# Kernel optimization log

Measured on AMD Instinct MI355X. Metric: run time of the kernel, lower is better.

## Reference

```python
import jax, jax.numpy as jnp
import numpy as np

B, S, D_IN, D_ATT = 8, 2048, 512, 512

def setup_inputs() -> dict:
    key = jax.random.key(0)
    ks = jax.random.split(key, 7)
    sc = 1.0 / np.sqrt(D_IN)
    return {
        "x": jax.random.normal(ks[0], (B, S, D_IN), dtype=jnp.float32),
        "Wq": jax.random.uniform(ks[1], (D_IN, D_ATT), jnp.float32, -sc, sc),
        "bq": jax.random.uniform(ks[2], (D_ATT,), jnp.float32, -sc, sc),
        "Wk": jax.random.uniform(ks[3], (D_IN, D_ATT), jnp.float32, -sc, sc),
        "bk": jax.random.uniform(ks[4], (D_ATT,), jnp.float32, -sc, sc),
        "Wv": jax.random.uniform(ks[5], (D_IN, D_ATT), jnp.float32, -sc, sc),
        "bv": jax.random.uniform(ks[6], (D_ATT,), jnp.float32, -sc, sc),
    }

def reference(x, Wq, bq, Wk, bk, Wv, bv):
    # Linear projections: [B, S, D_att]
    q = jnp.einsum("bsd,de->bse", x, Wq) + bq
    k = jnp.einsum("bsd,de->bse", x, Wk) + bk
    v = jnp.einsum("bsd,de->bse", x, Wv) + bv
    # Full scores matrix [B, S, S]; note: NO 1/sqrt(d) scaling in original.
    scores = jnp.einsum("bqe,bke->bqk", q, k)
    attn = jax.nn.softmax(scores, axis=-1)
    return jnp.einsum("bqk,bke->bqe", attn, v)
```

## Files before the change

kernel.cpp:

```cpp
#include <hip/hip_runtime.h>
#include <cstdint>
#include <cstddef>


#define SEQ 2048
#define DIM 512
#define NB 8
#define BSZ (NB * SEQ)
#define KT 64
#define NT (SEQ / KT)

typedef __attribute__((ext_vector_type(8))) _Float16 half8;
typedef __attribute__((ext_vector_type(4))) _Float16 half4;
typedef __attribute__((ext_vector_type(2))) __fp16 fp16x2;
typedef __attribute__((ext_vector_type(4))) float f32x4;
typedef __attribute__((ext_vector_type(16))) float f32x16;

__device__ __forceinline__ unsigned short f2h(float f) {
  _Float16 h = (_Float16)f;
  return __builtin_bit_cast(unsigned short, h);
}
__device__ __forceinline__ half8 ld_frag(const unsigned short* p) {
  return *(const half8*)(const void*)p;
}
__device__ __forceinline__ void gl_lds16(const unsigned short* g, unsigned short* l) {
  __builtin_amdgcn_global_load_lds(
      (__attribute__((address_space(1))) void*)g,
      (__attribute__((address_space(3))) void*)l, 16, 0, 0);
}
__device__ __forceinline__ void bar_vm0() {
  asm volatile("s_waitcnt vmcnt(0)\ns_barrier" ::: "memory");
}
__device__ __forceinline__ void bar_lgkm() {
  asm volatile("s_waitcnt lgkmcnt(0)\ns_barrier" ::: "memory");
}
__device__ __forceinline__ void bar_lgkm_vm0() {
  asm volatile("s_waitcnt lgkmcnt(0) vmcnt(0)\ns_barrier" ::: "memory");
}

__global__ __launch_bounds__(256) void cvt_x_kernel(
    const float* __restrict__ X, unsigned short* __restrict__ xh)
{
  size_t i0 = ((size_t)blockIdx.x * 256 + threadIdx.x) * 8;
  float4 a = *(const float4*)&X[i0];
  float4 b = *(const float4*)&X[i0 + 4];
  ushort4 o0; o0.x = f2h(a.x); o0.y = f2h(a.y); o0.z = f2h(a.z); o0.w = f2h(a.w);
  ushort4 o1; o1.x = f2h(b.x); o1.y = f2h(b.y); o1.z = f2h(b.z); o1.w = f2h(b.w);
  *(ushort4*)&xh[i0] = o0;
  *(ushort4*)&xh[i0 + 4] = o1;
}

__global__ __launch_bounds__(256) void cvt_w_kernel(
    const float* __restrict__ Wq, const float* __restrict__ Wk,
    const float* __restrict__ Wv, unsigned short* __restrict__ Wt)
{
  const int z = blockIdx.z;
  const float* W = (z == 0) ? Wq : (z == 1) ? Wk : Wv;
  unsigned short* out = Wt + (size_t)z * DIM * DIM;
  const int k0 = blockIdx.x * 64, n0 = blockIdx.y * 64;
  const int t = threadIdx.x;
  __shared__ unsigned short tl[64 * 72];
#pragma unroll
  for (int i = 0; i < 4; i++) {
    int f = t + 256 * i;
    int kr = f >> 4, c4 = (f & 15) * 4;
    float4 v = *(const float4*)&W[(size_t)(k0 + kr) * DIM + n0 + c4];
    tl[(c4 + 0) * 72 + kr] = f2h(v.x);
    tl[(c4 + 1) * 72 + kr] = f2h(v.y);
    tl[(c4 + 2) * 72 + kr] = f2h(v.z);
    tl[(c4 + 3) * 72 + kr] = f2h(v.w);
  }
  __syncthreads();
#pragma unroll
  for (int i = 0; i < 2; i++) {
    int f = t + 256 * i;
    int nr = f >> 3, k8 = (f & 7) * 8;
    *(uint4*)&out[(size_t)(n0 + nr) * DIM + k0 + k8] = *(const uint4*)&tl[nr * 72 + k8];
  }
}

__global__ __launch_bounds__(256) void proj_kernel(
    const unsigned short* __restrict__ xh, const unsigned short* __restrict__ Wt,
    const float* __restrict__ bq, const float* __restrict__ bk,
    const float* __restrict__ bv, unsigned short* __restrict__ outbase)
{
  const int z = blockIdx.z;
  const unsigned short* Wz = Wt + (size_t)z * DIM * DIM;
  const float* bias = (z == 0) ? bq : (z == 1) ? bk : bv;
  unsigned short* out = outbase + (size_t)z * BSZ * DIM;
  const int m0 = blockIdx.x * 128, n0 = blockIdx.y * 128;
  const int t = threadIdx.x, lane = t & 63, wave = t >> 6;
  const int wrow = (wave >> 1) * 64, wcol = (wave & 1) * 64;
  const int lr = lane & 15, lq = (lane >> 4) * 8;

  __shared__ unsigned short sm[128 * 132];
  unsigned short* As = sm;
  unsigned short* Bs = sm + 128 * 64;

  f32x4 acc[4][4];
  const f32x4 zero = {0.f, 0.f, 0.f, 0.f};
#pragma unroll
  for (int r = 0; r < 4; r++)
#pragma unroll
    for (int c = 0; c < 4; c++) acc[r][c] = zero;

  for (int k0 = 0; k0 < DIM; k0 += 64) {
    __syncthreads();
#pragma unroll
    for (int i = 0; i < 4; i++) {
      int f = t + 256 * i;
      int row = f >> 3, c8 = (f & 7) * 8;
      gl_lds16(&xh[(size_t)(m0 + row) * DIM + k0 + c8], &As[i * 2048 + wave * 512]);
      gl_lds16(&Wz[(size_t)(n0 + row) * DIM + k0 + c8], &Bs[i * 2048 + wave * 512]);
    }
    __syncthreads();
#pragma unroll
    for (int kk = 0; kk < 64; kk += 32) {
      half8 a[4], b[4];
#pragma unroll
      for (int r = 0; r < 4; r++) a[r] = ld_frag(&As[(wrow + 16 * r + lr) * 64 + kk + lq]);
#pragma unroll
      for (int c = 0; c < 4; c++) b[c] = ld_frag(&Bs[(wcol + 16 * c + lr) * 64 + kk + lq]);
#pragma unroll
      for (int r = 0; r < 4; r++)
#pragma unroll
        for (int c = 0; c < 4; c++)
          acc[r][c] = __builtin_amdgcn_mfma_f32_16x16x32_f16(a[r], b[c], acc[r][c], 0, 0, 0);
    }
  }
  __syncthreads();
#pragma unroll
  for (int c = 0; c < 4; c++) {
    float bb = bias[n0 + wcol + 16 * c + lr];
#pragma unroll
    for (int r = 0; r < 4; r++)
#pragma unroll
      for (int e = 0; e < 4; e++)
        sm[(wrow + 16 * r + (lane >> 4) * 4 + e) * 132 + wcol + 16 * c + lr] =
            f2h(acc[r][c][e] + bb);
  }
  __syncthreads();
#pragma unroll
  for (int i = 0; i < 8; i++) {
    int f = t + 256 * i;
    int row = f >> 4, c8 = (f & 15) * 8;
    *(uint4*)&out[(size_t)(m0 + row) * DIM + n0 + c8] = *(const uint4*)&sm[row * 132 + c8];
  }
}

__global__ __launch_bounds__(256) void vtrans_kernel(
    const unsigned short* __restrict__ vh, unsigned short* __restrict__ vt)
{
  const int b = blockIdx.z;
  const int s0 = blockIdx.x * 64, n0 = blockIdx.y * 64;
  const int t = threadIdx.x;
  __shared__ unsigned short tl[64 * 72];
#pragma unroll
  for (int i = 0; i < 2; i++) {
    int f = t + 256 * i;
    int sr = f >> 3, c8 = (f & 7) * 8;
    uint4 raw = *(const uint4*)&vh[((size_t)b * SEQ + s0 + sr) * DIM + n0 + c8];
    unsigned short u[8];
    *(uint4*)u = raw;
#pragma unroll
    for (int j = 0; j < 8; j++) tl[(c8 + j) * 72 + sr] = u[j];
  }
  __syncthreads();
#pragma unroll
  for (int i = 0; i < 2; i++) {
    int f = t + 256 * i;
    int nr = f >> 3, s8 = (f & 7) * 8;
    *(uint4*)&vt[((size_t)b * DIM + n0 + nr) * SEQ + s0 + s8] = *(const uint4*)&tl[nr * 72 + s8];
  }
}

#define PSTR 68
#define OSTR 516

__global__ __launch_bounds__(256, 1) void flash_kernel(
    const unsigned short* __restrict__ Qb, const unsigned short* __restrict__ Kb,
    const unsigned short* __restrict__ Vtb, float* __restrict__ Ob)
{
  const int zb = blockIdx.x & 7;
  const int q0 = (blockIdx.x >> 3) * 64;
  const unsigned short* Q = Qb + (size_t)zb * SEQ * DIM;
  const unsigned short* K = Kb + (size_t)zb * SEQ * DIM;
  const unsigned short* V = Vtb + (size_t)zb * DIM * SEQ;
  float* Out = Ob + (size_t)zb * SEQ * DIM;

  const int t = threadIdx.x, lane = t & 63, wave = t >> 6;
  const int l31 = lane & 31, hi = lane >> 5;
  const int kh = wave & 1, rh = wave >> 1;
  const int lr = lane & 15, lq4 = lane >> 4;
  const float L2E = 1.4426950408889634f;

  __shared__ unsigned short lds[70664];
  unsigned short* Qbuf = lds;
  unsigned short* Kbuf = lds + 32768;
  unsigned short* Pbuf = lds + 65536;
  float* mpart = (float*)(lds + 65536 + 64 * PSTR);
  float* lpart = mpart + 128;
  float* abuf = lpart + 128;
  float* lrun = abuf + 64;
  unsigned int* fbuf = (unsigned int*)(lrun + 64);

  if (t < 64) lrun[t] = 0.f;

  int koff[16];
#pragma unroll
  for (int i = 0; i < 16; i++) {
    int f = t + 256 * i;
    int row = f >> 6, c = f & 63;
    koff[i] = row * DIM + (c ^ (row & 7)) * 8;
  }

#pragma unroll
  for (int i = 0; i < 16; i++)
    gl_lds16(&Q[(size_t)q0 * DIM + koff[i]], &Qbuf[i * 2048 + wave * 512]);
#pragma unroll
  for (int i = 0; i < 16; i++)
    gl_lds16(&K[koff[i]], &Kbuf[i * 2048 + wave * 512]);

  f32x4 acc[32];
  const f32x4 zero = {0.f, 0.f, 0.f, 0.f};
#pragma unroll
  for (int ob = 0; ob < 32; ob++) acc[ob] = zero;
  float m_run = -__builtin_inff();

  const int keyrow = kh * 32 + l31, ksw = keyrow & 7;
  const int qrow = rh * 32 + l31, qsw = qrow & 7;
  const unsigned short* Kc = Kbuf + keyrow * 512;
  const unsigned short* Qc = Qbuf + qrow * 512;

  for (int kt = 0; kt < NT; kt++) {
    bar_vm0();

    const unsigned short* Vb = V + (size_t)(wave * 128 + lr) * SEQ + kt * KT + lq4 * 8;
    half8 vfA[8];
#pragma unroll
    for (int dc = 0; dc < 4; dc++)
#pragma unroll
      for (int ks = 0; ks < 2; ks++)
        vfA[dc * 2 + ks] = ld_frag(Vb + (size_t)dc * 16 * SEQ + ks * 32);

    f32x16 s0 = {0.f, 0.f, 0.f, 0.f, 0.f, 0.f, 0.f, 0.f,
                 0.f, 0.f, 0.f, 0.f, 0.f, 0.f, 0.f, 0.f};
    f32x16 s1 = s0;
    __builtin_amdgcn_s_setprio(1);
#pragma unroll
    for (int j = 0; j < 16; j++) {
      half8 kf0 = ld_frag(&Kc[((2 * j + hi) ^ ksw) << 3]);
      half8 qv0 = ld_frag(&Qc[((2 * j + hi) ^ qsw) << 3]);
      half8 kf1 = ld_frag(&Kc[((2 * (j + 16) + hi) ^ ksw) << 3]);
      half8 qv1 = ld_frag(&Qc[((2 * (j + 16) + hi) ^ qsw) << 3]);
      s0 = __builtin_amdgcn_mfma_f32_32x32x16_f16(kf0, qv0, s0, 0, 0, 0);
      s1 = __builtin_amdgcn_mfma_f32_32x32x16_f16(kf1, qv1, s1, 0, 0, 0);
    }
    __builtin_amdgcn_s_setprio(0);
    f32x16 sacc = s0 + s1;

    float mx = sacc[0];
#pragma unroll
    for (int i2 = 1; i2 < 16; i2++) mx = fmaxf(mx, sacc[i2]);
    mx = fmaxf(mx, __shfl_xor(mx, 32, 64));
    if (lane < 32) mpart[kh * 64 + rh * 32 + lane] = mx;
    bar_lgkm();

    if (kt + 1 < NT) {
      const unsigned short* Kt = K + (size_t)(kt + 1) * KT * DIM;
#pragma unroll
      for (int i = 0; i < 16; i++)
        gl_lds16(&Kt[koff[i]], &Kbuf[i * 2048 + wave * 512]);
    }
    half8 vfB[8];
#pragma unroll
    for (int dc = 0; dc < 4; dc++)
#pragma unroll
      for (int ks = 0; ks < 2; ks++)
        vfB[dc * 2 + ks] = ld_frag(Vb + (size_t)(dc + 4) * 16 * SEQ + ks * 32);

    float mo = mpart[(kh ^ 1) * 64 + rh * 32 + l31];
    float mxc = fmaxf(mx, mo);
    bool keep = (mxc - m_run <= 8.0f);
    float mnew = keep ? m_run : mxc;
    float alpha = keep ? 1.0f : exp2f((m_run - mnew) * L2E);
    m_run = mnew;
    if (kh == 0 && lane < 32) abuf[rh * 32 + lane] = alpha;
    unsigned long long ball = __ballot(keep);
    if (lane == 0) fbuf[wave] = (ball == ~0ull) ? 1u : 0u;

    float psum = 0.f;
#pragma unroll
    for (int w2 = 0; w2 < 4; w2++) {
      float p0 = exp2f((sacc[4 * w2 + 0] - mnew) * L2E);
      float p1 = exp2f((sacc[4 * w2 + 1] - mnew) * L2E);
      float p2 = exp2f((sacc[4 * w2 + 2] - mnew) * L2E);
      float p3 = exp2f((sacc[4 * w2 + 3] - mnew) * L2E);
      psum += (p0 + p1) + (p2 + p3);
      fp16x2 pa = __builtin_amdgcn_cvt_pkrtz(p0, p1);
      fp16x2 pb = __builtin_amdgcn_cvt_pkrtz(p2, p3);
      unsigned long long both =
          ((unsigned long long)__builtin_bit_cast(unsigned int, pb) << 32) |
          __builtin_bit_cast(unsigned int, pa);
      *(unsigned long long*)&Pbuf[qrow * PSTR + kh * 32 + w2 * 8 + 4 * hi] = both;
    }
    psum += __shfl_xor(psum, 32, 64);
    if (lane < 32) lpart[kh * 64 + rh * 32 + lane] = psum;
    bar_lgkm();
    if (kh == 0 && lane < 32) {
      int r = rh * 32 + lane;
      lrun[r] = alpha * lrun[r] + lpart[r] + lpart[64 + r];
    }

    if (!(fbuf[0] & fbuf[1] & fbuf[2] & fbuf[3])) {
#pragma unroll
      for (int rg = 0; rg < 4; rg++)
#pragma unroll
        for (int e = 0; e < 4; e++) {
          float a = abuf[rg * 16 + lq4 * 4 + e];
#pragma unroll
          for (int dc = 0; dc < 8; dc++) acc[rg * 8 + dc][e] *= a;
        }
    }

    half8 pf[4][2];
#pragma unroll
    for (int rg = 0; rg < 4; rg++)
#pragma unroll
      for (int ks = 0; ks < 2; ks++) {
        const unsigned short* pp = &Pbuf[(rg * 16 + lr) * PSTR + ks * 32 + lq4 * 8];
        half4 lo = *(const half4*)(const void*)pp;
        half4 h2 = *(const half4*)(const void*)(pp + 4);
        half8 v;
#pragma unroll
        for (int q = 0; q < 4; q++) { v[q] = lo[q]; v[4 + q] = h2[q]; }
        pf[rg][ks] = v;
      }
    __builtin_amdgcn_s_setprio(1);
#pragma unroll
    for (int dc = 0; dc < 4; dc++)
#pragma unroll
      for (int rg = 0; rg < 4; rg++) {
        acc[rg * 8 + dc] =
            __builtin_amdgcn_mfma_f32_16x16x32_f16(pf[rg][0], vfA[dc * 2 + 0],
                                                   acc[rg * 8 + dc], 0, 0, 0);
        acc[rg * 8 + dc] =
            __builtin_amdgcn_mfma_f32_16x16x32_f16(pf[rg][1], vfA[dc * 2 + 1],
                                                   acc[rg * 8 + dc], 0, 0, 0);
      }
#pragma unroll
    for (int dc = 4; dc < 8; dc++)
#pragma unroll
      for (int rg = 0; rg < 4; rg++) {
        acc[rg * 8 + dc] =
            __builtin_amdgcn_mfma_f32_16x16x32_f16(pf[rg][0], vfB[(dc - 4) * 2 + 0],
                                                   acc[rg * 8 + dc], 0, 0, 0);
        acc[rg * 8 + dc] =
            __builtin_amdgcn_mfma_f32_16x16x32_f16(pf[rg][1], vfB[(dc - 4) * 2 + 1],
                                                   acc[rg * 8 + dc], 0, 0, 0);
      }
    __builtin_amdgcn_s_setprio(0);
  }

  bar_lgkm_vm0();

  float linv[4][4];
#pragma unroll
  for (int rg = 0; rg < 4; rg++)
#pragma unroll
    for (int e = 0; e < 4; e++) linv[rg][e] = 1.0f / lrun[rg * 16 + lq4 * 4 + e];

  float* Obuf = (float*)lds;
#pragma unroll
  for (int h = 0; h < 2; h++) {
    __syncthreads();
#pragma unroll
    for (int r2 = 0; r2 < 2; r2++) {
      int rg = h * 2 + r2;
#pragma unroll
      for (int e = 0; e < 4; e++) {
        int rowh = r2 * 16 + lq4 * 4 + e;
#pragma unroll
        for (int dc = 0; dc < 8; dc++)
          Obuf[rowh * OSTR + wave * 128 + dc * 16 + lr] = acc[rg * 8 + dc][e] * linv[rg][e];
      }
    }
    __syncthreads();
#pragma unroll
    for (int i = 0; i < 16; i++) {
      int f = t + 256 * i;
      int rowh = f >> 7, c4 = (f & 127) * 4;
      *(float4*)&Out[(size_t)(q0 + h * 32 + rowh) * DIM + c4] =
          *(const float4*)&Obuf[rowh * OSTR + c4];
    }
  }
}

extern "C" void kernel_launch(void* const* d_in, const int* in_sizes, int n_in,
                              void* d_out, int out_size, void* d_ws, size_t ws_size,
                              hipStream_t stream)
{
  const float* X  = (const float*)d_in[0];
  const float* Wq = (const float*)d_in[1];
  const float* bq = (const float*)d_in[2];
  const float* Wk = (const float*)d_in[3];
  const float* bk = (const float*)d_in[4];
  const float* Wv = (const float*)d_in[5];
  const float* bv = (const float*)d_in[6];
  float* Out = (float*)d_out;

  char* ws = (char*)d_ws;
  const size_t MB = 1u << 20;
  unsigned short* qh = (unsigned short*)(ws);
  unsigned short* kh = (unsigned short*)(ws + 16 * MB);
  unsigned short* vh = (unsigned short*)(ws + 32 * MB);
  unsigned short* vt = (unsigned short*)(ws + 48 * MB);
  unsigned short* xh = (unsigned short*)(ws + 48 * MB);
  unsigned short* Wt = (unsigned short*)(ws + 64 * MB);

  cvt_x_kernel<<<dim3(BSZ * DIM / 2048), 256, 0, stream>>>(X, xh);
  cvt_w_kernel<<<dim3(8, 8, 3), 256, 0, stream>>>(Wq, Wk, Wv, Wt);
  proj_kernel<<<dim3(BSZ / 128, DIM / 128, 3), 256, 0, stream>>>(
      xh, Wt, bq, bk, bv, qh);
  vtrans_kernel<<<dim3(SEQ / 64, DIM / 64, NB), 256, 0, stream>>>(vh, vt);
  flash_kernel<<<dim3(NB * SEQ / 64), 256, 0, stream>>>(qh, kh, vt, Out);
}
```

Before: 293.2 us.

## Warp-specialize flash kernel into QK/softmax and PV wave groups with double-buffered P

Doubles the block to 512 threads and splits the waves into two groups. Four waves compute QK scores and the softmax for tile r, while the other four do the PV MFMAs for tile r-1, reading P, alpha and partial sums from double-buffered LDS. The goal is to overlap the softmax and exp work with the PV matrix multiplies instead of running them back to back. It also drops the lazy-rescale threshold and the skip flag, so the accumulator is rescaled every step, and it costs more LDS, more registers per block and one extra pipeline iteration.

```diff
diff --git a/kernel.cpp b/kernel.cpp
--- a/kernel.cpp
+++ b/kernel.cpp
@@ -9,6 +9,7 @@
 #define BSZ (NB * SEQ)
 #define KT 64
 #define NT (SEQ / KT)
+#define QROWS 64
 
 typedef __attribute__((ext_vector_type(8))) _Float16 half8;
 typedef __attribute__((ext_vector_type(4))) _Float16 half4;
@@ -27,9 +28,6 @@
   __builtin_amdgcn_global_load_lds(
       (__attribute__((address_space(1))) void*)g,
       (__attribute__((address_space(3))) void*)l, 16, 0, 0);
-}
-__device__ __forceinline__ void bar_vm0() {
-  asm volatile("s_waitcnt vmcnt(0)\ns_barrier" ::: "memory");
 }
 __device__ __forceinline__ void bar_lgkm() {
   asm volatile("s_waitcnt lgkmcnt(0)\ns_barrier" ::: "memory");
@@ -177,12 +175,12 @@
 #define PSTR 68
 #define OSTR 516
 
-__global__ __launch_bounds__(256, 1) void flash_kernel(
+__global__ __launch_bounds__(512, 1) void flash_kernel(
     const unsigned short* __restrict__ Qb, const unsigned short* __restrict__ Kb,
     const unsigned short* __restrict__ Vtb, float* __restrict__ Ob)
 {
   const int zb = blockIdx.x & 7;
-  const int q0 = (blockIdx.x >> 3) * 64;
+  const int q0 = (blockIdx.x >> 3) * QROWS;
   const unsigned short* Q = Qb + (size_t)zb * SEQ * DIM;
   const unsigned short* K = Kb + (size_t)zb * SEQ * DIM;
   const unsigned short* V = Vtb + (size_t)zb * DIM * SEQ;
@@ -190,41 +188,45 @@
 
   const int t = threadIdx.x, lane = t & 63, wave = t >> 6;
   const int l31 = lane & 31, hi = lane >> 5;
-  const int kh = wave & 1, rh = wave >> 1;
+  const int kh = wave & 1, rh = (wave >> 1) & 1;
+  const int yw = wave & 3;
   const int lr = lane & 15, lq4 = lane >> 4;
   const float L2E = 1.4426950408889634f;
 
-  __shared__ unsigned short lds[70664];
+  __shared__ unsigned short lds[75264];
   unsigned short* Qbuf = lds;
   unsigned short* Kbuf = lds + 32768;
   unsigned short* Pbuf = lds + 65536;
-  float* mpart = (float*)(lds + 65536 + 64 * PSTR);
-  float* lpart = mpart + 128;
-  float* abuf = lpart + 128;
-  float* lrun = abuf + 64;
-  unsigned int* fbuf = (unsigned int*)(lrun + 64);
-
-  if (t < 64) lrun[t] = 0.f;
+  float* mpart = (float*)(lds + 65536 + 2 * 64 * PSTR);
+  float* abuf  = mpart + 128;
+  float* lpart = abuf + 128;
 
   int koff[16];
 #pragma unroll
   for (int i = 0; i < 16; i++) {
-    int f = t + 256 * i;
+    int f = (t & 255) + 256 * i;
     int row = f >> 6, c = f & 63;
     koff[i] = row * DIM + (c ^ (row & 7)) * 8;
   }
 
-#pragma unroll
-  for (int i = 0; i < 16; i++)
-    gl_lds16(&Q[(size_t)q0 * DIM + koff[i]], &Qbuf[i * 2048 + wave * 512]);
-#pragma unroll
-  for (int i = 0; i < 16; i++)
-    gl_lds16(&K[koff[i]], &Kbuf[i * 2048 + wave * 512]);
+  if (wave < 4) {
+#pragma unroll
+    for (int i = 0; i < 16; i++)
+      gl_lds16(&Q[(size_t)q0 * DIM + koff[i]], &Qbuf[i * 2048 + wave * 512]);
+#pragma unroll
+    for (int i = 0; i < 16; i++)
+      gl_lds16(&K[koff[i]], &Kbuf[i * 2048 + wave * 512]);
+  }
 
   f32x4 acc[32];
   const f32x4 zero = {0.f, 0.f, 0.f, 0.f};
 #pragma unroll
   for (int ob = 0; ob < 32; ob++) acc[ob] = zero;
+  float l_y[4][4];
+#pragma unroll
+  for (int rg = 0; rg < 4; rg++)
+#pragma unroll
+    for (int e = 0; e < 4; e++) l_y[rg][e] = 0.f;
   float m_run = -__builtin_inff();
 
   const int keyrow = kh * 32 + l31, ksw = keyrow & 7;
@@ -232,163 +234,168 @@
   const unsigned short* Kc = Kbuf + keyrow * 512;
   const unsigned short* Qc = Qbuf + qrow * 512;
 
-  for (int kt = 0; kt < NT; kt++) {
-    bar_vm0();
-
-    const unsigned short* Vb = V + (size_t)(wave * 128 + lr) * SEQ + kt * KT + lq4 * 8;
-    half8 vfA[8];
-#pragma unroll
-    for (int dc = 0; dc < 4; dc++)
-#pragma unroll
-      for (int ks = 0; ks < 2; ks++)
-        vfA[dc * 2 + ks] = ld_frag(Vb + (size_t)dc * 16 * SEQ + ks * 32);
-
-    f32x16 s0 = {0.f, 0.f, 0.f, 0.f, 0.f, 0.f, 0.f, 0.f,
-                 0.f, 0.f, 0.f, 0.f, 0.f, 0.f, 0.f, 0.f};
-    f32x16 s1 = s0;
-    __builtin_amdgcn_s_setprio(1);
-#pragma unroll
-    for (int j = 0; j < 16; j++) {
-      half8 kf0 = ld_frag(&Kc[((2 * j + hi) ^ ksw) << 3]);
-      half8 qv0 = ld_frag(&Qc[((2 * j + hi) ^ qsw) << 3]);
-      half8 kf1 = ld_frag(&Kc[((2 * (j + 16) + hi) ^ ksw) << 3]);
-      half8 qv1 = ld_frag(&Qc[((2 * (j + 16) + hi) ^ qsw) << 3]);
-      s0 = __builtin_amdgcn_mfma_f32_32x32x16_f16(kf0, qv0, s0, 0, 0, 0);
-      s1 = __builtin_amdgcn_mfma_f32_32x32x16_f16(kf1, qv1, s1, 0, 0, 0);
-    }
-    __builtin_amdgcn_s_setprio(0);
-    f32x16 sacc = s0 + s1;
-
-    float mx = sacc[0];
-#pragma unroll
-    for (int i2 = 1; i2 < 16; i2++) mx = fmaxf(mx, sacc[i2]);
-    mx = fmaxf(mx, __shfl_xor(mx, 32, 64));
-    if (lane < 32) mpart[kh * 64 + rh * 32 + lane] = mx;
+  for (int r = 0; r <= NT; r++) {
+    bar_lgkm_vm0();
+
+    f32x16 sacc;
+    float mx = 0.f;
+    half8 vf[16];
+    half8 pf[4][2];
+
+    if (wave < 4) {
+      if (r < NT) {
+        f32x16 s0c = {0.f, 0.f, 0.f, 0.f, 0.f, 0.f, 0.f, 0.f,
+                      0.f, 0.f, 0.f, 0.f, 0.f, 0.f, 0.f, 0.f};
+        f32x16 s1c = s0c;
+        __builtin_amdgcn_s_setprio(1);
+#pragma unroll
+        for (int j = 0; j < 16; j++) {
+          half8 kf0 = ld_frag(&Kc[((2 * j + hi) ^ ksw) << 3]);
+          half8 qv0 = ld_frag(&Qc[((2 * j + hi) ^ qsw) << 3]);
+          half8 kf1 = ld_frag(&Kc[((2 * (j + 16) + hi) ^ ksw) << 3]);
+          half8 qv1 = ld_frag(&Qc[((2 * (j + 16) + hi) ^ qsw) << 3]);
+          s0c = __builtin_amdgcn_mfma_f32_32x32x16_f16(kf0, qv0, s0c, 0, 0, 0);
+          s1c = __builtin_amdgcn_mfma_f32_32x32x16_f16(kf1, qv1, s1c, 0, 0, 0);
+        }
+        __builtin_amdgcn_s_setprio(0);
+        sacc = s0c + s1c;
+        mx = sacc[0];
+#pragma unroll
+        for (int i2 = 1; i2 < 16; i2++) mx = fmaxf(mx, sacc[i2]);
+        mx = fmaxf(mx, __shfl_xor(mx, 32, 64));
+        if (lane < 32) mpart[kh * 64 + rh * 32 + lane] = mx;
+      }
+    } else {
+      if (r > 0) {
+        const int pb = (r - 1) & 1;
+        const unsigned short* Vb =
+            V + (size_t)(yw * 128 + lr) * SEQ + (size_t)(r - 1) * KT + lq4 * 8;
+#pragma unroll
+        for (int dc = 0; dc < 8; dc++)
+#pragma unroll
+          for (int ks = 0; ks < 2; ks++)
+            vf[dc * 2 + ks] = ld_frag(Vb + (size_t)dc * 16 * SEQ + ks * 32);
+#pragma unroll
+        for (int rg = 0; rg < 4; rg++)
+#pragma unroll
+          for (int e = 0; e < 4; e++) {
+            int row = rg * 16 + lq4 * 4 + e;
+            float a = abuf[pb * 64 + row];
+            float ls = lpart[pb * 128 + row] + lpart[pb * 128 + 64 + row];
+            l_y[rg][e] = a * l_y[rg][e] + ls;
+#pragma unroll
+            for (int dc = 0; dc < 8; dc++) acc[rg * 8 + dc][e] *= a;
+          }
+#pragma unroll
+        for (int rg = 0; rg < 4; rg++)
+#pragma unroll
+          for (int ks = 0; ks < 2; ks++) {
+            const unsigned short* pp =
+                &Pbuf[pb * 64 * PSTR + (rg * 16 + lr) * PSTR + ks * 32 + lq4 * 8];
+            half4 lo = *(const half4*)(const void*)pp;
+            half4 h2 = *(const half4*)(const void*)(pp + 4);
+            half8 v;
+#pragma unroll
+            for (int q = 0; q < 4; q++) { v[q] = lo[q]; v[4 + q] = h2[q]; }
+            pf[rg][ks] = v;
+          }
+        __builtin_amdgcn_s_setprio(1);
+#pragma unroll
+        for (int dc = 0; dc < 4; dc++)
+#pragma unroll
+          for (int rg = 0; rg < 4; rg++) {
+            acc[rg * 8 + dc] = __builtin_amdgcn_mfma_f32_16x16x32_f16(
+                pf[rg][0], vf[dc * 2 + 0], acc[rg * 8 + dc], 0, 0, 0);
+            acc[rg * 8 + dc] = __builtin_amdgcn_mfma_f32_16x16x32_f16(
+                pf[rg][1], vf[dc * 2 + 1], acc[rg * 8 + dc], 0, 0, 0);
+          }
+        __builtin_amdgcn_s_setprio(0);
+      }
+    }
+
     bar_lgkm();
 
-    if (kt + 1 < NT) {
-      const unsigned short* Kt = K + (size_t)(kt + 1) * KT * DIM;
-#pragma unroll
-      for (int i = 0; i < 16; i++)
-        gl_lds16(&Kt[koff[i]], &Kbuf[i * 2048 + wave * 512]);
-    }
-    half8 vfB[8];
-#pragma unroll
-    for (int dc = 0; dc < 4; dc++)
-#pragma unroll
-      for (int ks = 0; ks < 2; ks++)
-        vfB[dc * 2 + ks] = ld_frag(Vb + (size_t)(dc + 4) * 16 * SEQ + ks * 32);
-
-    float mo = mpart[(kh ^ 1) * 64 + rh * 32 + l31];
-    float mxc = fmaxf(mx, mo);
-    bool keep = (mxc - m_run <= 8.0f);
-    float mnew = keep ? m_run : mxc;
-    float alpha = keep ? 1.0f : exp2f((m_run - mnew) * L2E);
-    m_run = mnew;
-    if (kh == 0 && lane < 32) abuf[rh * 32 + lane] = alpha;
-    unsigned long long ball = __ballot(keep);
-    if (lane == 0) fbuf[wave] = (ball == ~0ull) ? 1u : 0u;
-
-    float psum = 0.f;
-#pragma unroll
-    for (int w2 = 0; w2 < 4; w2++) {
-      float p0 = exp2f((sacc[4 * w2 + 0] - mnew) * L2E);
-      float p1 = exp2f((sacc[4 * w2 + 1] - mnew) * L2E);
-      float p2 = exp2f((sacc[4 * w2 + 2] - mnew) * L2E);
-      float p3 = exp2f((sacc[4 * w2 + 3] - mnew) * L2E);
-      psum += (p0 + p1) + (p2 + p3);
-      fp16x2 pa = __builtin_amdgcn_cvt_pkrtz(p0, p1);
-      fp16x2 pb = __builtin_amdgcn_cvt_pkrtz(p2, p3);
-      unsigned long long both =
-          ((unsigned long long)__builtin_bit_cast(unsigned int, pb) << 32) |
-          __builtin_bit_cast(unsigned int, pa);
-      *(unsigned long long*)&Pbuf[qrow * PSTR + kh * 32 + w2 * 8 + 4 * hi] = both;
-    }
-    psum += __shfl_xor(psum, 32, 64);
-    if (lane < 32) lpart[kh * 64 + rh * 32 + lane] = psum;
-    bar_lgkm();
-    if (kh == 0 && lane < 32) {
-      int r = rh * 32 + lane;
-      lrun[r] = alpha * lrun[r] + lpart[r] + lpart[64 + r];
-    }
-
-    if (!(fbuf[0] & fbuf[1] & fbuf[2] & fbuf[3])) {
-#pragma unroll
-      for (int rg = 0; rg < 4; rg++)
-#pragma unroll
-        for (int e = 0; e < 4; e++) {
-          float a = abuf[rg * 16 + lq4 * 4 + e];
-#pragma unroll
-          for (int dc = 0; dc < 8; dc++) acc[rg * 8 + dc][e] *= a;
+    if (wave < 4) {
+      if (r + 1 < NT) {
+        const unsigned short* Kt = K + (size_t)(r + 1) * KT * DIM;
+#pragma unroll
+        for (int i = 0; i < 16; i++)
+          gl_lds16(&Kt[koff[i]], &Kbuf[i * 2048 + wave * 512]);
+      }
+      if (r < NT) {
+        const int rb = r & 1;
+        float mo = mpart[(kh ^ 1) * 64 + rh * 32 + l31];
+        float mnew = fmaxf(m_run, fmaxf(mx, mo));
+        float alpha = exp2f((m_run - mnew) * L2E);
+        m_run = mnew;
+        if (kh == 0 && lane < 32) abuf[rb * 64 + rh * 32 + lane] = alpha;
+        float psum = 0.f;
+#pragma unroll
+        for (int w2 = 0; w2 < 4; w2++) {
+          float p0 = exp2f((sacc[4 * w2 + 0] - mnew) * L2E);
+          float p1 = exp2f((sacc[4 * w2 + 1] - mnew) * L2E);
+          float p2 = exp2f((sacc[4 * w2 + 2] - mnew) * L2E);
+          float p3 = exp2f((sacc[4 * w2 + 3] - mnew) * L2E);
+          psum += (p0 + p1) + (p2 + p3);
+          fp16x2 pa = __builtin_amdgcn_cvt_pkrtz(p0, p1);
+          fp16x2 pb2 = __builtin_amdgcn_cvt_pkrtz(p2, p3);
+          unsigned long long both =
+              ((unsigned long long)__builtin_bit_cast(unsigned int, pb2) << 32) |
+              __builtin_bit_cast(unsigned int, pa);
+          *(unsigned long long*)&Pbuf[rb * 64 * PSTR + qrow * PSTR + kh * 32 +
+                                      w2 * 8 + 4 * hi] = both;
         }
-    }
-
-    half8 pf[4][2];
+        psum += __shfl_xor(psum, 32, 64);
+        if (lane < 32) lpart[rb * 128 + kh * 64 + rh * 32 + lane] = psum;
+      }
+    } else {
+      if (r > 0) {
+        __builtin_amdgcn_s_setprio(1);
+#pragma unroll
+        for (int dc = 4; dc < 8; dc++)
+#pragma unroll
+          for (int rg = 0; rg < 4; rg++) {
+            acc[rg * 8 + dc] = __builtin_amdgcn_mfma_f32_16x16x32_f16(
+                pf[rg][0], vf[dc * 2 + 0], acc[rg * 8 + dc], 0, 0, 0);
+            acc[rg * 8 + dc] = __builtin_amdgcn_mfma_f32_16x16x32_f16(
+                pf[rg][1], vf[dc * 2 + 1], acc[rg * 8 + dc], 0, 0, 0);
+          }
+        __builtin_amdgcn_s_setprio(0);
+      }
+    }
+  }
+
+  bar_lgkm_vm0();
+
+  float linv[4][4];
+  if (wave >= 4) {
 #pragma unroll
     for (int rg = 0; rg < 4; rg++)
 #pragma unroll
-      for (int ks = 0; ks < 2; ks++) {
-        const unsigned short* pp = &Pbuf[(rg * 16 + lr) * PSTR + ks * 32 + lq4 * 8];
-        half4 lo = *(const half4*)(const void*)pp;
-        half4 h2 = *(const half4*)(const void*)(pp + 4);
-        half8 v;
-#pragma unroll
-        for (int q = 0; q < 4; q++) { v[q] = lo[q]; v[4 + q] = h2[q]; }
-        pf[rg][ks] = v;
-      }
-    __builtin_amdgcn_s_setprio(1);
-#pragma unroll
-    for (int dc = 0; dc < 4; dc++)
-#pragma unroll
-      for (int rg = 0; rg < 4; rg++) {
-        acc[rg * 8 + dc] =
-            __builtin_amdgcn_mfma_f32_16x16x32_f16(pf[rg][0], vfA[dc * 2 + 0],
-                                                   acc[rg * 8 + dc], 0, 0, 0);
-        acc[rg * 8 + dc] =
-            __builtin_amdgcn_mfma_f32_16x16x32_f16(pf[rg][1], vfA[dc * 2 + 1],
-                                                   acc[rg * 8 + dc], 0, 0, 0);
-      }
-#pragma unroll
-    for (int dc = 4; dc < 8; dc++)
-#pragma unroll
-      for (int rg = 0; rg < 4; rg++) {
-        acc[rg * 8 + dc] =
-            __builtin_amdgcn_mfma_f32_16x16x32_f16(pf[rg][0], vfB[(dc - 4) * 2 + 0],
-                                                   acc[rg * 8 + dc], 0, 0, 0);
-        acc[rg * 8 + dc] =
-            __builtin_amdgcn_mfma_f32_16x16x32_f16(pf[rg][1], vfB[(dc - 4) * 2 + 1],
-                                                   acc[rg * 8 + dc], 0, 0, 0);
-      }
-    __builtin_amdgcn_s_setprio(0);
-  }
-
-  bar_lgkm_vm0();
-
-  float linv[4][4];
-#pragma unroll
-  for (int rg = 0; rg < 4; rg++)
-#pragma unroll
-    for (int e = 0; e < 4; e++) linv[rg][e] = 1.0f / lrun[rg * 16 + lq4 * 4 + e];
-
+      for (int e = 0; e < 4; e++) linv[rg][e] = 1.0f / l_y[rg][e];
+  }
   float* Obuf = (float*)lds;
 #pragma unroll
   for (int h = 0; h < 2; h++) {
     __syncthreads();
-#pragma unroll
-    for (int r2 = 0; r2 < 2; r2++) {
-      int rg = h * 2 + r2;
-#pragma unroll
-      for (int e = 0; e < 4; e++) {
-        int rowh = r2 * 16 + lq4 * 4 + e;
-#pragma unroll
-        for (int dc = 0; dc < 8; dc++)
-          Obuf[rowh * OSTR + wave * 128 + dc * 16 + lr] = acc[rg * 8 + dc][e] * linv[rg][e];
+    if (wave >= 4) {
+#pragma unroll
+      for (int r2 = 0; r2 < 2; r2++) {
+        int rg = h * 2 + r2;
+#pragma unroll
+        for (int e = 0; e < 4; e++) {
+          int rowh = r2 * 16 + lq4 * 4 + e;
+#pragma unroll
+          for (int dc = 0; dc < 8; dc++)
+            Obuf[rowh * OSTR + yw * 128 + dc * 16 + lr] =
+                acc[rg * 8 + dc][e] * linv[rg][e];
+        }
       }
     }
     __syncthreads();
 #pragma unroll
-    for (int i = 0; i < 16; i++) {
-      int f = t + 256 * i;
+    for (int i = 0; i < 8; i++) {
+      int f = t + 512 * i;
       int rowh = f >> 7, c4 = (f & 127) * 4;
       *(float4*)&Out[(size_t)(q0 + h * 32 + rowh) * DIM + c4] =
           *(const float4*)&Obuf[rowh * OSTR + c4];
@@ -423,5 +430,5 @@
   proj_kernel<<<dim3(BSZ / 128, DIM / 128, 3), 256, 0, stream>>>(
       xh, Wt, bq, bk, bv, qh);
   vtrans_kernel<<<dim3(SEQ / 64, DIM / 64, NB), 256, 0, stream>>>(vh, vt);
-  flash_kernel<<<dim3(NB * SEQ / 64), 256, 0, stream>>>(qh, kh, vt, Out);
-}
+  flash_kernel<<<dim3(NB * SEQ / QROWS), 512, 0, stream>>>(qh, kh, vt, Out);
+}
```

Result: slower. 786.4 us (+168.2%).
